# Kernel optimization log

Hardware: AMD Instinct MI355X
Metric: run time of the kernel (lower is better)

Reference implementation:

```python
import jax, jax.numpy as jnp
import numpy as np

B, S, H, L, C = 32, 512, 768, 512, 3  # batch, seq, hidden, max_length, num_classes


def _lin_init(k, fan_in, shape):
    return jax.random.normal(k, shape, jnp.float32) * (1.0 / np.sqrt(fan_in))


def setup_inputs() -> dict:
    key = jax.random.key(0)
    ks = jax.random.split(key, 18)
    return {
        "tokens": jax.random.normal(ks[0], (B, S, H), jnp.float32),
        # shared Q/K/V projections (used for both token- and feature-attention)
        "Wq": _lin_init(ks[1], H, (H, H)), "bq": jnp.zeros((H,), jnp.float32),
        "Wk": _lin_init(ks[2], H, (H, H)), "bk": jnp.zeros((H,), jnp.float32),
        "Wv": _lin_init(ks[3], H, (H, H)), "bv": jnp.zeros((H,), jnp.float32),
        # TSGSA: Linear(H,1)+ReLU gate over tokens
        "W_ts": _lin_init(ks[4], H, (H, 1)), "b_ts": jnp.zeros((1,), jnp.float32),
        # FSGSA: Linear(max_length,1)+ReLU gate over padded seq axis (also reused for FGSA per source bug)
        "W_fs": _lin_init(ks[5], L, (L, 1)), "b_fs": jnp.zeros((1,), jnp.float32),
        # TGSA: Linear(H,H)+Sigmoid gate
        "W_tg": _lin_init(ks[6], H, (H, H)), "b_tg": jnp.zeros((H,), jnp.float32),
        # fnn: Linear(7H,H) -> Linear(H,C)
        "W1": _lin_init(ks[7], 7 * H, (7 * H, H)), "b1": jnp.zeros((H,), jnp.float32),
        "W2": _lin_init(ks[8], H, (H, C)), "b2": jnp.zeros((C,), jnp.float32),
    }


def _ln(x):
    # LayerNorm over (seq, hidden) jointly, eps=1e-8; freshly-instantiated affine params are identity
    m = jnp.mean(x, axis=(1, 2), keepdims=True)
    v = jnp.var(x, axis=(1, 2), keepdims=True)
    return (x - m) * jax.lax.rsqrt(v + 1e-8)


def reference(tokens, Wq, bq, Wk, bk, Wv, bv, W_ts, b_ts, W_fs, b_fs, W_tg, b_tg, W1, b1, W2, b2):
    scale = 1.0 / np.sqrt(H)
    Q = tokens @ Wq + bq  # [B,S,H]
    K = tokens @ Wk + bk
    V = tokens @ Wv + bv
    # token-direction self-attention: softmax(Q K^T / sqrt(H)) V
    att = jax.nn.softmax(jnp.einsum('bsh,bth->bst', Q, K) * scale, axis=-1)  # [B,S,S]
    TSA = jnp.einsum('bst,bth->bsh', att, V)
    # feature-direction self-attention: V @ softmax(Q^T K / sqrt(H))
    attN = jax.nn.softmax(jnp.einsum('bsh,bsg->bhg', Q, K) * scale, axis=-1)  # [B,H,H]
    FSA = jnp.einsum('bsh,bhg->bsg', V, attN)
    # gate branches
    TSGSA = jax.nn.relu(tokens @ W_ts + b_ts) * tokens  # [B,S,1]*[B,S,H]
    tpad = jnp.pad(tokens.transpose(0, 2, 1), ((0, 0), (0, 0), (0, L - S)))  # [B,H,L]
    gate_f = jax.nn.relu(tpad @ W_fs + b_fs)  # [B,H,1]
    FSGSA = (gate_f * tokens.transpose(0, 2, 1)).transpose(0, 2, 1)  # [B,S,H]
    TGSA = jax.nn.sigmoid(tokens @ W_tg + b_tg) * tokens
    FGSA = FSGSA  # source bug: FGSA branch applies self.FSGSA, identical to FSGSA
    out_all = jnp.concatenate(
        [tokens, _ln(TSA), _ln(FSA), _ln(TGSA), _ln(FGSA), _ln(TSGSA), _ln(FSGSA)], axis=2)  # [B,S,7H]
    pooled = jnp.mean(out_all, axis=1)  # [B,7H]
    return (pooled @ W1 + b1) @ W2 + b2  # [B,C]
```

## Files before the change

### kernel.cpp

```cpp
#include <hip/hip_runtime.h>
#include <cmath>

typedef unsigned short u16;
typedef __attribute__((ext_vector_type(4))) float f32x4;
typedef __attribute__((ext_vector_type(4))) unsigned int u32x4;
typedef __attribute__((ext_vector_type(8))) __bf16 bf16x8;

__device__ __forceinline__ u16 f2b(float f) {
  unsigned int u = __builtin_bit_cast(unsigned int, f);
  return (u16)((u + 0x7fffu + ((u >> 16) & 1u)) >> 16);
}
__device__ __forceinline__ float b2f(u16 h) {
  unsigned int u = ((unsigned int)h) << 16;
  return __builtin_bit_cast(float, u);
}

__device__ __forceinline__ void glds16(const u16* g, u16* l) {
  __builtin_amdgcn_global_load_lds(
      (const __attribute__((address_space(1))) void*)g,
      (__attribute__((address_space(3))) void*)l, 16, 0, 0);
}

template <int EPI>
__global__ __launch_bounds__(512) void gemm_f_k(
    const u16* __restrict__ Ap, const u16* __restrict__ Bp, u16* __restrict__ Cp,
    u16* __restrict__ CpT, const float* __restrict__ bias,
    const u16* __restrict__ tokp, float* __restrict__ colsum,
    float* __restrict__ bstat, const float* __restrict__ rs, int K, int lda,
    int ldb, int ldc, long sA, long sB, long sC, float scale) {
  __shared__ alignas(16) u16 Asm[2][8192];
  __shared__ alignas(16) u16 Bsm[2][4096];
  __shared__ float scol_s[128];
  __shared__ float scrow[256];
  __shared__ float sred[2];

  const int gx = gridDim.x, gxy = gx * gridDim.y;
  const int nwg = gxy * gridDim.z;
  int orig = (blockIdx.z * gridDim.y + blockIdx.y) * gx + blockIdx.x;
  int gwi = (orig & 7) * (nwg >> 3) + (orig >> 3);
  const int z = gwi / gxy;
  int rem = gwi - z * gxy;
  const int ty = rem / gx, tx = rem - ty * gx;
  const int tileM = ty << 8, tileN = tx << 7;

  const u16* Abase = Ap + (size_t)z * sA;
  const u16* Bbase = Bp + (size_t)z * sB;

  const int tid = threadIdx.x;
  const int lane = tid & 63, w = tid >> 6;
  const int wr = (w >> 1) << 6, wc = (w & 1) << 6;
  const int fr = lane & 15, fg = lane >> 4;

  f32x4 acc[4][4];
#pragma unroll
  for (int i = 0; i < 4; ++i)
#pragma unroll
    for (int j = 0; j < 4; ++j) acc[i][j] = (f32x4){0.f, 0.f, 0.f, 0.f};

  const int sArow = (w << 5) + (lane >> 2);
  const int sBrow = (w << 4) + (lane >> 2);
  const int scol = (((lane & 3) ^ ((lane >> 3) & 3)) << 3);
  const u16* gA = Abase + (size_t)(tileM + sArow) * lda + scol;
  const u16* gB = Bbase + (size_t)(tileN + sBrow) * ldb + scol;
  const int ldsA = (w << 5) * 32;
  const int ldsB = (w << 4) * 32;

  auto STAGE = [&](int buf, int k0) {
    glds16(gA + k0, &Asm[buf][ldsA]);
    glds16(gA + (size_t)16 * lda + k0, &Asm[buf][ldsA + 512]);
    glds16(gB + k0, &Bsm[buf][ldsB]);
  };

  const int col_off = ((fg ^ ((fr >> 1) & 3)) << 3);

  const int nt = K >> 5;
  STAGE(0, 0);
  int cur = 0;
  for (int t = 0; t < nt; ++t) {
    if (t + 1 < nt) {
      STAGE(cur ^ 1, (t + 1) << 5);
      asm volatile("s_waitcnt vmcnt(3)" ::: "memory");
    } else {
      asm volatile("s_waitcnt vmcnt(0)" ::: "memory");
    }
    __builtin_amdgcn_s_barrier();
    asm volatile("" ::: "memory");
    const u16* Ab = Asm[cur];
    const u16* Bb = Bsm[cur];
    bf16x8 av[4], bw[4];
#pragma unroll
    for (int m = 0; m < 4; ++m)
      av[m] = *(const bf16x8*)&Ab[(wr + (m << 4) + fr) * 32 + col_off];
#pragma unroll
    for (int n = 0; n < 4; ++n)
      bw[n] = *(const bf16x8*)&Bb[(wc + (n << 4) + fr) * 32 + col_off];
#pragma unroll
    for (int m = 0; m < 4; ++m)
#pragma unroll
      for (int n = 0; n < 4; ++n)
        acc[m][n] =
            __builtin_amdgcn_mfma_f32_16x16x32_bf16(av[m], bw[n], acc[m][n], 0, 0, 0);
    asm volatile("" ::: "memory");
    __builtin_amdgcn_s_barrier();
    cur ^= 1;
  }

  if constexpr (EPI == 0) {
    const int cbuf = tileN / 768;
    const int nbase = tileN - cbuf * 768;
    u16* Cz = Cp + (size_t)cbuf * sC;
#pragma unroll
    for (int m = 0; m < 4; ++m) {
#pragma unroll
      for (int n = 0; n < 4; ++n) {
        const int gcol = tileN + wc + (n << 4) + fr;
        const int lcol = nbase + wc + (n << 4) + fr;
        const float bv2 = bias[gcol];
#pragma unroll
        for (int r = 0; r < 4; ++r) {
          const int grow = tileM + wr + (m << 4) + (fg << 2) + r;
          Cz[(size_t)grow * 768 + lcol] = f2b(acc[m][n][r] + bv2);
        }
      }
    }
    u16* Ct = CpT + (size_t)cbuf * sC;
    const int zb = tileM >> 9;
    const int sbase = tileM & 511;
#pragma unroll
    for (int m = 0; m < 4; ++m) {
#pragma unroll
      for (int n = 0; n < 4; ++n) {
        const int gcol = tileN + wc + (n << 4) + fr;
        const int lcol = nbase + wc + (n << 4) + fr;
        const int srow0 = sbase + wr + (m << 4) + (fg << 2);
        union { u16 u[4]; unsigned long long q; } pk;
#pragma unroll
        for (int r = 0; r < 4; ++r) pk.u[r] = f2b(acc[m][n][r] + bias[gcol]);
        *(unsigned long long*)&Ct[((size_t)(zb * 768 + lcol) << 9) + srow0] = pk.q;
      }
    }
  } else if constexpr (EPI == 1) {
    if (tid < 128) scol_s[tid] = 0.f;
    if (tid == 0) { sred[0] = 0.f; sred[1] = 0.f; }
    __syncthreads();
    float ls = 0.f, lq = 0.f;
#pragma unroll
    for (int n = 0; n < 4; ++n) {
      float cpart = 0.f;
      const int gcol = tileN + wc + (n << 4) + fr;
      const float bv2 = bias[gcol];
#pragma unroll
      for (int m = 0; m < 4; ++m) {
#pragma unroll
        for (int r = 0; r < 4; ++r) {
          const int grow = tileM + wr + (m << 4) + (fg << 2) + r;
          float g = 1.f / (1.f + __expf(-(acc[m][n][r] + bv2)));
          float v = g * b2f(tokp[(size_t)grow * 768 + gcol]);
          cpart += v; ls += v; lq += v * v;
        }
      }
      atomicAdd(&scol_s[wc + (n << 4) + fr], cpart);
    }
    atomicAdd(&sred[0], ls);
    atomicAdd(&sred[1], lq);
    __syncthreads();
    const int b = tileM >> 9;
    if (tid < 128) atomicAdd(&colsum[(size_t)b * 768 + tileN + tid], scol_s[tid]);
    if (tid == 0) {
      atomicAdd(&bstat[b], sred[0]);
      atomicAdd(&bstat[32 + b], sred[1]);
    }
  } else if constexpr (EPI == 4) {
    u16* Cz = Cp + (size_t)z * sC;
    float lsum[4];
#pragma unroll
    for (int n = 0; n < 4; ++n) {
      const int gcol = tileN + wc + (n << 4) + fr;
      float s2 = 0.f;
#pragma unroll
      for (int m = 0; m < 4; ++m) {
#pragma unroll
        for (int r = 0; r < 4; ++r) {
          const int grow = tileM + wr + (m << 4) + (fg << 2) + r;
          float e = __expf(acc[m][n][r] * scale);
          Cz[(size_t)grow * ldc + gcol] = f2b(e);
          s2 += e;
        }
      }
      lsum[n] = s2;
    }
    float* red = (float*)&Asm[0][0];
    const int slot = ((w >> 1) << 2) + fg;
    __syncthreads();
#pragma unroll
    for (int n = 0; n < 4; ++n)
      red[slot * 132 + wc + (n << 4) + fr] = lsum[n];
    __syncthreads();
    if (tid < 128) {
      float s2 = 0.f;
#pragma unroll
      for (int i = 0; i < 16; ++i) s2 += red[i * 132 + tid];
      const int ty3 = tileM >> 8;
      colsum[((size_t)z * 3 + ty3) * 768 + tileN + tid] = s2;
    }
  } else if constexpr (EPI == 5) {
    u16* Cz = Cp + (size_t)z * sC;
    if (tid < 256) scrow[tid] = 0.f;
    __syncthreads();
    float rpart[4][4];
#pragma unroll
    for (int m = 0; m < 4; ++m)
#pragma unroll
      for (int r = 0; r < 4; ++r) rpart[m][r] = 0.f;
#pragma unroll
    for (int n = 0; n < 4; ++n) {
      const int gcol = tileN + wc + (n << 4) + fr;
#pragma unroll
      for (int m = 0; m < 4; ++m) {
#pragma unroll
        for (int r = 0; r < 4; ++r) {
          const int grow = tileM + wr + (m << 4) + (fg << 2) + r;
          float e = __expf(acc[m][n][r] * scale);
          Cz[(size_t)grow * ldc + gcol] = f2b(e);
          rpart[m][r] += e;
        }
      }
    }
#pragma unroll
    for (int m = 0; m < 4; ++m) {
#pragma unroll
      for (int r = 0; r < 4; ++r) {
        float v = rpart[m][r];
        v += __shfl_xor(v, 1); v += __shfl_xor(v, 2);
        v += __shfl_xor(v, 4); v += __shfl_xor(v, 8);
        if (fr == 0) atomicAdd(&scrow[wr + (m << 4) + (fg << 2) + r], v);
      }
    }
    __syncthreads();
    if (tid < 256) atomicAdd(&colsum[(size_t)z * 512 + tileM + tid], scrow[tid]);
  } else if constexpr (EPI == 6) {
    float isr[4][4];
#pragma unroll
    for (int m = 0; m < 4; ++m)
#pragma unroll
      for (int r = 0; r < 4; ++r)
        isr[m][r] =
            1.f / rs[(size_t)z * 512 + tileM + wr + (m << 4) + (fg << 2) + r];
    if (tid < 128) scol_s[tid] = 0.f;
    if (tid == 0) { sred[0] = 0.f; sred[1] = 0.f; }
    __syncthreads();
    float ls = 0.f, lq = 0.f;
#pragma unroll
    for (int n = 0; n < 4; ++n) {
      float cpart = 0.f;
#pragma unroll
      for (int m = 0; m < 4; ++m) {
#pragma unroll
        for (int r = 0; r < 4; ++r) {
          float v = acc[m][n][r] * isr[m][r];
          cpart += v; ls += v; lq += v * v;
        }
      }
      atomicAdd(&scol_s[wc + (n << 4) + fr], cpart);
    }
    atomicAdd(&sred[0], ls);
    atomicAdd(&sred[1], lq);
    __syncthreads();
    if (tid < 128) atomicAdd(&colsum[(size_t)z * 768 + tileN + tid], scol_s[tid]);
    if (tid == 0) {
      atomicAdd(&bstat[z], sred[0]);
      atomicAdd(&bstat[32 + z], sred[1]);
    }
  } else {
    if (tid < 128) scol_s[tid] = 0.f;
    if (tid == 0) { sred[0] = 0.f; sred[1] = 0.f; }
    __syncthreads();
    float ls = 0.f, lq = 0.f;
#pragma unroll
    for (int n = 0; n < 4; ++n) {
      float cpart = 0.f;
#pragma unroll
      for (int m = 0; m < 4; ++m) {
#pragma unroll
        for (int r = 0; r < 4; ++r) {
          float v = acc[m][n][r];
          cpart += v; ls += v; lq += v * v;
        }
      }
      atomicAdd(&scol_s[wc + (n << 4) + fr], cpart);
    }
    atomicAdd(&sred[0], ls);
    atomicAdd(&sred[1], lq);
    __syncthreads();
    if (tid < 128) atomicAdd(&colsum[(size_t)z * 768 + tileN + tid], scol_s[tid]);
    if (tid == 0) {
      atomicAdd(&bstat[z], sred[0]);
      atomicAdd(&bstat[32 + z], sred[1]);
    }
  }
}

__global__ __launch_bounds__(256) void cvt_row_k(
    const float* __restrict__ tok, u16* __restrict__ tokb,
    const float* __restrict__ Wts, const float* __restrict__ bts,
    float* __restrict__ gate_t, float* __restrict__ rowsum,
    float* __restrict__ rowsumsq) {
  const int w = threadIdx.x >> 6, lane = threadIdx.x & 63;
  const int row = blockIdx.x * 4 + w;
  const float* p = tok + (size_t)row * 768;
  u16* q = tokb + (size_t)row * 768;
  float s = 0.f, sq = 0.f, g = 0.f;
#pragma unroll
  for (int i = 0; i < 3; ++i) {
    const int idx = (i * 64 + lane) << 2;
    f32x4 v = *(const f32x4*)(p + idx);
    f32x4 wv = *(const f32x4*)(Wts + idx);
    union { u16 u[4]; unsigned long long q8; } pk;
#pragma unroll
    for (int j = 0; j < 4; ++j) {
      s += v[j]; sq += v[j] * v[j]; g += v[j] * wv[j];
      pk.u[j] = f2b(v[j]);
    }
    *(unsigned long long*)(q + idx) = pk.q8;
  }
#pragma unroll
  for (int o = 32; o > 0; o >>= 1) {
    s += __shfl_xor(s, o); sq += __shfl_xor(sq, o); g += __shfl_xor(g, o);
  }
  if (lane == 0) {
    gate_t[row] = fmaxf(g + bts[0], 0.f);
    rowsum[row] = s;
    rowsumsq[row] = sq;
  }
}

__global__ __launch_bounds__(256) void transpose_w4_k(
    const float* __restrict__ W0, const float* __restrict__ W1,
    const float* __restrict__ W2, const float* __restrict__ W3,
    u16* __restrict__ WT) {
  const float* W = blockIdx.z == 0 ? W0 : blockIdx.z == 1 ? W1
                   : blockIdx.z == 2 ? W2 : W3;
  u16* dst = WT + (size_t)blockIdx.z * 589824;
  __shared__ float t[64][65];
  const int r0 = blockIdx.y << 6, c0 = blockIdx.x << 6;
  for (int i = threadIdx.x; i < 4096; i += 256) {
    int r = i >> 6, c = i & 63;
    t[r][c] = W[(size_t)(r0 + r) * 768 + c0 + c];
  }
  __syncthreads();
  for (int i = threadIdx.x; i < 4096; i += 256) {
    int rr = i >> 6, cc = i & 63;
    dst[(size_t)(c0 + rr) * 768 + r0 + cc] = f2b(t[cc][rr]);
  }
}

__global__ __launch_bounds__(256) void v2scale_k(const u16* __restrict__ Vb,
                                                 const float* __restrict__ psum,
                                                 u16* __restrict__ V2) {
  __shared__ float inv[768];
  const int z = blockIdx.x, sb = blockIdx.y;
  const float* pz = psum + (size_t)z * 2304;
  for (int h = threadIdx.x; h < 768; h += 256)
    inv[h] = 1.f / (pz[h] + pz[h + 768] + pz[h + 1536]);
  __syncthreads();
  const size_t base = (size_t)z * 393216 + (size_t)sb * 64 * 768;
  for (int i = 0; i < 24; ++i) {
    const int u = i * 256 + threadIdx.x;
    const int row = u / 96, seg = (u - row * 96) * 8;
    const size_t idx = base + (size_t)row * 768 + seg;
    union { u32x4 q; u16 us[8]; } in, ot;
    in.q = *(const u32x4*)&Vb[idx];
#pragma unroll
    for (int j = 0; j < 8; ++j) ot.us[j] = f2b(b2f(in.us[j]) * inv[seg + j]);
    *(u32x4*)&V2[idx] = ot.q;
  }
}

__global__ __launch_bounds__(256) void col_stats_k(
    const u16* __restrict__ tokb, const float* __restrict__ Wfs,
    const float* __restrict__ bfs, const float* __restrict__ gate_t,
    float* __restrict__ gate_f, float* __restrict__ colsum_tok,
    float* __restrict__ colsumsq_tok, float* __restrict__ colsum_tsg) {
  const int b = blockIdx.x, h = blockIdx.y * 256 + threadIdx.x;
  const u16* p = tokb + (size_t)b * 512 * 768 + h;
  const float* gt = gate_t + b * 512;
  float cs = 0.f, cq = 0.f, gf = 0.f, tg = 0.f;
#pragma unroll 4
  for (int s = 0; s < 512; ++s) {
    float t = b2f(p[(size_t)s * 768]);
    cs += t; cq += t * t; gf += t * Wfs[s]; tg += t * gt[s];
  }
  const int idx = b * 768 + h;
  gate_f[idx] = fmaxf(gf + bfs[0], 0.f);
  colsum_tok[idx] = cs;
  colsumsq_tok[idx] = cq;
  colsum_tsg[idx] = tg;
}

__global__ __launch_bounds__(256) void batch_stats_k(
    const float* __restrict__ gate_t, const float* __restrict__ rowsum,
    const float* __restrict__ rowsumsq, const float* __restrict__ gate_f,
    const float* __restrict__ colsum_tok, const float* __restrict__ colsumsq_tok,
    float* __restrict__ st) {
  __shared__ float red[4][256];
  const int b = blockIdx.x, tid = threadIdx.x;
  float ts = 0.f, tq = 0.f, fs = 0.f, fq = 0.f;
  for (int s = tid; s < 512; s += 256) {
    float g = gate_t[b * 512 + s];
    ts += g * rowsum[b * 512 + s];
    tq += g * g * rowsumsq[b * 512 + s];
  }
  for (int h = tid; h < 768; h += 256) {
    float g = gate_f[b * 768 + h];
    fs += g * colsum_tok[b * 768 + h];
    fq += g * g * colsumsq_tok[b * 768 + h];
  }
  red[0][tid] = ts; red[1][tid] = tq; red[2][tid] = fs; red[3][tid] = fq;
  __syncthreads();
  for (int o = 128; o > 0; o >>= 1) {
    if (tid < o) {
      red[0][tid] += red[0][tid + o];
      red[1][tid] += red[1][tid + o];
      red[2][tid] += red[2][tid + o];
      red[3][tid] += red[3][tid + o];
    }
    __syncthreads();
  }
  if (tid == 0) {
    st[b] = red[0][0]; st[32 + b] = red[1][0];
    st[64 + b] = red[2][0]; st[96 + b] = red[3][0];
  }
}

__global__ __launch_bounds__(768) void pooled_k(
    const float* __restrict__ colsum_tok, const float* __restrict__ colsum_tsa,
    const float* __restrict__ bstat_tsa, const float* __restrict__ colsum_fsa,
    const float* __restrict__ bstat_fsa, const float* __restrict__ colsum_tgsa,
    const float* __restrict__ bstat_tgsa, const float* __restrict__ colsum_tsg,
    const float* __restrict__ gate_f, const float* __restrict__ st,
    float* __restrict__ pooled) {
  const int b = blockIdx.x, h = threadIdx.x;
  const float invS = 1.f / 512.f, invN = 1.f / (512.f * 768.f);
  const int i = b * 768 + h;
  float* pr = pooled + (size_t)b * 5376;
  pr[h] = colsum_tok[i] * invS;
  auto lnslot = [&](int slot, float cs, float bs, float bq) {
    float m = bs * invN;
    float var = bq * invN - m * m;
    pr[slot * 768 + h] = (cs * invS - m) * rsqrtf(var + 1e-8f);
  };
  lnslot(1, colsum_tsa[i], bstat_tsa[b], bstat_tsa[32 + b]);
  lnslot(2, colsum_fsa[i], bstat_fsa[b], bstat_fsa[32 + b]);
  lnslot(3, colsum_tgsa[i], bstat_tgsa[b], bstat_tgsa[32 + b]);
  const float fsg_cs = gate_f[i] * colsum_tok[i];
  lnslot(4, fsg_cs, st[64 + b], st[96 + b]);
  lnslot(5, colsum_tsg[i], st[b], st[32 + b]);
  lnslot(6, fsg_cs, st[64 + b], st[96 + b]);
}

__global__ __launch_bounds__(256) void fnn1_k(const float* __restrict__ pooled,
                                              const float* __restrict__ W1,
                                              float* __restrict__ tmp1) {
  __shared__ float sp[128][36];
  const int c0 = blockIdx.x << 7, k0 = blockIdx.y << 7;
  const int tid = threadIdx.x;
  for (int i = tid; i < 4096; i += 256) {
    int b = i >> 7, j = i & 127;
    sp[j][b] = pooled[(size_t)b * 5376 + k0 + j];
  }
  __syncthreads();
  const int c = c0 + (tid & 127);
  const int u = (tid >> 7) << 4;
  float acc[16];
#pragma unroll
  for (int t = 0; t < 16; ++t) acc[t] = 0.f;
#pragma unroll 4
  for (int j = 0; j < 128; ++j) {
    float w = W1[(size_t)(k0 + j) * 768 + c];
    const f32x4* row = (const f32x4*)&sp[j][u];
#pragma unroll
    for (int t4 = 0; t4 < 4; ++t4) {
      f32x4 v = row[t4];
#pragma unroll
      for (int r = 0; r < 4; ++r) acc[t4 * 4 + r] += v[r] * w;
    }
  }
#pragma unroll
  for (int t = 0; t < 16; ++t) atomicAdd(&tmp1[(u + t) * 768 + c], acc[t]);
}

__global__ __launch_bounds__(256) void fnn2_k(const float* __restrict__ tmp1,
                                              const float* __restrict__ b1,
                                              const float* __restrict__ W2,
                                              const float* __restrict__ b2,
                                              float* __restrict__ out) {
  const int gw = blockIdx.x * 4 + (threadIdx.x >> 6);
  const int lane = threadIdx.x & 63;
  const int b = gw / 3, c = gw % 3;
  float a = 0.f;
#pragma unroll
  for (int i = 0; i < 12; ++i) {
    int k = lane + i * 64;
    a += (tmp1[b * 768 + k] + b1[k]) * W2[k * 3 + c];
  }
#pragma unroll
  for (int o = 32; o > 0; o >>= 1) a += __shfl_xor(a, o);
  if (lane == 0) out[b * 3 + c] = a + b2[c];
}

extern "C" void kernel_launch(void* const* d_in, const int* in_sizes, int n_in,
                              void* d_out, int out_size, void* d_ws, size_t ws_size,
                              hipStream_t stream) {
  const float* tokens = (const float*)d_in[0];
  const float* Wq = (const float*)d_in[1];
  const float* bq = (const float*)d_in[2];
  const float* Wk = (const float*)d_in[3];
  const float* bk = (const float*)d_in[4];
  const float* Wv = (const float*)d_in[5];
  const float* bv = (const float*)d_in[6];
  const float* Wts = (const float*)d_in[7];
  const float* bts = (const float*)d_in[8];
  const float* Wfs = (const float*)d_in[9];
  const float* bfs = (const float*)d_in[10];
  const float* Wtg = (const float*)d_in[11];
  const float* btg = (const float*)d_in[12];
  const float* W1 = (const float*)d_in[13];
  const float* b1 = (const float*)d_in[14];
  const float* W2 = (const float*)d_in[15];
  const float* b2 = (const float*)d_in[16];
  float* out = (float*)d_out;

  char* ws = (char*)d_ws;
  size_t off = 0;
  auto take = [&](size_t bytes) -> char* {
    char* p = ws + off;
    off += (bytes + 255) & ~(size_t)255;
    return p;
  };
  u16* tokb = (u16*)take((size_t)16384 * 768 * 2);
  u16* WqT = (u16*)take((size_t)768 * 768 * 2);
  u16* WkT = (u16*)take((size_t)768 * 768 * 2);
  u16* WvT = (u16*)take((size_t)768 * 768 * 2);
  u16* WtgT = (u16*)take((size_t)768 * 768 * 2);
  u16* Qb = (u16*)take((size_t)16384 * 768 * 2);
  u16* Kb = (u16*)take((size_t)16384 * 768 * 2);
  u16* Vb = (u16*)take((size_t)16384 * 768 * 2);
  u16* Qt = (u16*)take((size_t)32 * 768 * 512 * 2);
  u16* Kt = (u16*)take((size_t)32 * 768 * 512 * 2);
  u16* Vt = (u16*)take((size_t)32 * 768 * 512 * 2);
  u16* attb = (u16*)take((size_t)32 * 512 * 512 * 2);
  u16* attNt = (u16*)take((size_t)32 * 768 * 768 * 2);
  float* bias3 = (float*)take(2304 * 4);
  float* psum = (float*)take((size_t)32 * 3 * 768 * 4);
  u16* V2 = Qt;
  char* zbase = ws + off;
  float* colsum_tsa = (float*)take(24576 * 4);
  float* colsum_fsa = (float*)take(24576 * 4);
  float* colsum_tgsa = (float*)take(24576 * 4);
  float* bstat_tsa = (float*)take(64 * 4);
  float* bstat_fsa = (float*)take(64 * 4);
  float* bstat_tgsa = (float*)take(64 * 4);
  float* rowsumE = (float*)take((size_t)32 * 512 * 4);
  float* tmp1 = (float*)take((size_t)32 * 768 * 4);
  size_t zbytes = (size_t)((ws + off) - zbase);
  float* colsum_tsg = (float*)take(24576 * 4);
  float* gate_t = (float*)take(16384 * 4);
  float* rowsum = (float*)take(16384 * 4);
  float* rowsumsq = (float*)take(16384 * 4);
  float* gate_f = (float*)take(24576 * 4);
  float* colsum_tok = (float*)take(24576 * 4);
  float* colsumsq_tok = (float*)take(24576 * 4);
  float* st4 = (float*)take(128 * 4);
  float* pooled = (float*)take((size_t)32 * 5376 * 4);

  hipMemsetAsync(zbase, 0, zbytes, stream);
  hipMemcpyAsync(bias3, bq, 768 * 4, hipMemcpyDeviceToDevice, stream);
  hipMemcpyAsync(bias3 + 768, bk, 768 * 4, hipMemcpyDeviceToDevice, stream);
  hipMemcpyAsync(bias3 + 1536, bv, 768 * 4, hipMemcpyDeviceToDevice, stream);

  const float scale = 1.0f / sqrtf(768.0f);
  const dim3 blk(256);
  const dim3 blk512(512);

  cvt_row_k<<<4096, blk, 0, stream>>>(tokens, tokb, Wts, bts, gate_t, rowsum,
                                      rowsumsq);
  transpose_w4_k<<<dim3(12, 12, 4), blk, 0, stream>>>(Wq, Wk, Wv, Wtg, WqT);

  gemm_f_k<0><<<dim3(18, 64, 1), blk512, 0, stream>>>(
      tokb, WqT, Qb, Qt, bias3, nullptr, nullptr, nullptr, nullptr, 768, 768,
      768, 768, 0, 0, 12582912, 0.f);
  gemm_f_k<1><<<dim3(6, 64, 1), blk512, 0, stream>>>(
      tokb, WtgT, nullptr, nullptr, btg, tokb, colsum_tgsa, bstat_tgsa, nullptr,
      768, 768, 768, 0, 0, 0, 0, 0.f);

  gemm_f_k<4><<<dim3(6, 3, 32), blk512, 0, stream>>>(
      Kt, Qt, attNt, nullptr, nullptr, nullptr, psum, nullptr, nullptr, 512,
      512, 512, 768, 393216, 393216, 589824, scale);
  v2scale_k<<<dim3(32, 8), blk, 0, stream>>>(Vb, psum, V2);

  gemm_f_k<5><<<dim3(4, 2, 32), blk512, 0, stream>>>(
      Qb, Kb, attb, nullptr, nullptr, nullptr, rowsumE, nullptr, nullptr, 768,
      768, 768, 512, 393216, 393216, 262144, scale);

  gemm_f_k<6><<<dim3(6, 2, 32), blk512, 0, stream>>>(
      attb, Vt, nullptr, nullptr, nullptr, nullptr, colsum_tsa, bstat_tsa,
      rowsumE, 512, 512, 512, 0, 262144, 393216, 0, 0.f);
  gemm_f_k<3><<<dim3(6, 2, 32), blk512, 0, stream>>>(
      V2, attNt, nullptr, nullptr, nullptr, nullptr, colsum_fsa, bstat_fsa,
      nullptr, 768, 768, 768, 0, 393216, 589824, 0, 0.f);

  col_stats_k<<<dim3(32, 3), blk, 0, stream>>>(tokb, Wfs, bfs, gate_t, gate_f,
                                               colsum_tok, colsumsq_tok, colsum_tsg);
  batch_stats_k<<<32, blk, 0, stream>>>(gate_t, rowsum, rowsumsq, gate_f,
                                        colsum_tok, colsumsq_tok, st4);

  pooled_k<<<32, 768, 0, stream>>>(colsum_tok, colsum_tsa, bstat_tsa, colsum_fsa,
                                   bstat_fsa, colsum_tgsa, bstat_tgsa, colsum_tsg,
                                   gate_f, st4, pooled);
  fnn1_k<<<dim3(6, 42), blk, 0, stream>>>(pooled, W1, tmp1);
  fnn2_k<<<24, blk, 0, stream>>>(tmp1, b1, W2, b2, out);
}
```

Baseline: 386.3 us.

## Add 256x256-tile QKV projection GEMM with 4-stage LDS pipeline

Replaces the generic EPI==0 QKV projection GEMM with a dedicated kernel that uses 256x256 output tiles (8x4 MFMA fragments per wave), a 4-deep global_load_lds ring buffer with explicit vmcnt waits, and raised wave priority around the MFMA block. Larger tiles raise arithmetic intensity and cut redundant global/LDS traffic. The deeper prefetch is meant to hide memory latency. The cost is more accumulator registers and 128KB of LDS per block, which lowers occupancy. The grid also drops to 576 blocks, which may leave some CUs unevenly loaded.

```diff
diff --git a/kernel.cpp b/kernel.cpp
--- a/kernel.cpp
+++ b/kernel.cpp
@@ -19,6 +19,122 @@
   __builtin_amdgcn_global_load_lds(
       (const __attribute__((address_space(1))) void*)g,
       (__attribute__((address_space(3))) void*)l, 16, 0, 0);
+}
+
+__global__ __launch_bounds__(512) void gemm_w_k(
+    const u16* __restrict__ Ap, const u16* __restrict__ Bp, u16* __restrict__ Cp,
+    u16* __restrict__ CpT, const float* __restrict__ bias, int K, int lda,
+    int ldb, long sC) {
+  __shared__ alignas(16) u16 smem[4][16384];
+
+  const int gx = gridDim.x;
+  const int nwg = gx * gridDim.y;
+  int orig = blockIdx.y * gx + blockIdx.x;
+  int gwi = (orig & 7) * (nwg >> 3) + (orig >> 3);
+  const int ty = gwi / gx, tx = gwi - ty * gx;
+  const int tileM = ty << 8, tileN = tx << 8;
+
+  const int tid = threadIdx.x;
+  const int lane = tid & 63, w = tid >> 6;
+  const int wm = (w >> 2) << 7;
+  const int wn = (w & 3) << 6;
+  const int fr = lane & 15, fg = lane >> 4;
+
+  f32x4 acc[8][4];
+#pragma unroll
+  for (int i = 0; i < 8; ++i)
+#pragma unroll
+    for (int j = 0; j < 4; ++j) acc[i][j] = (f32x4){0.f, 0.f, 0.f, 0.f};
+
+  const int r1 = tid >> 2, c1 = tid & 3;
+  const int r2 = r1 + 128;
+  const int sc1 = ((c1 ^ ((r1 >> 1) & 3)) << 3);
+  const int sc2 = ((c1 ^ ((r2 >> 1) & 3)) << 3);
+  const u16* gA1 = Ap + (size_t)(tileM + r1) * lda + sc1;
+  const u16* gA2 = Ap + (size_t)(tileM + r2) * lda + sc2;
+  const u16* gB1 = Bp + (size_t)(tileN + r1) * ldb + sc1;
+  const u16* gB2 = Bp + (size_t)(tileN + r2) * ldb + sc2;
+
+  auto STAGE = [&](int buf, int k0) {
+    u16* base = &smem[buf][0];
+    glds16(gA1 + k0, base + tid * 8);
+    glds16(gA2 + k0, base + (tid + 512) * 8);
+    glds16(gB1 + k0, base + 8192 + tid * 8);
+    glds16(gB2 + k0, base + 8192 + (tid + 512) * 8);
+  };
+  const int col_off = ((fg ^ ((fr >> 1) & 3)) << 3);
+
+  const int nt = K >> 5;
+  STAGE(0, 0);
+  STAGE(1, 32);
+  STAGE(2, 64);
+  asm volatile("s_waitcnt vmcnt(8)" ::: "memory");
+  __builtin_amdgcn_s_barrier();
+  for (int t = 0; t < nt; ++t) {
+    asm volatile("" ::: "memory");
+    if (t + 3 < nt) STAGE((t + 3) & 3, (t + 3) << 5);
+    const u16* Ab = &smem[t & 3][0];
+    const u16* Bb = &smem[t & 3][8192];
+    bf16x8 av[8], bw[4];
+#pragma unroll
+    for (int m = 0; m < 8; ++m)
+      av[m] = *(const bf16x8*)&Ab[(wm + (m << 4) + fr) * 32 + col_off];
+#pragma unroll
+    for (int n = 0; n < 4; ++n)
+      bw[n] = *(const bf16x8*)&Bb[(wn + (n << 4) + fr) * 32 + col_off];
+    __builtin_amdgcn_s_setprio(1);
+#pragma unroll
+    for (int m = 0; m < 8; ++m)
+#pragma unroll
+      for (int n = 0; n < 4; ++n)
+        acc[m][n] =
+            __builtin_amdgcn_mfma_f32_16x16x32_bf16(av[m], bw[n], acc[m][n], 0, 0, 0);
+    __builtin_amdgcn_s_setprio(0);
+    asm volatile("" ::: "memory");
+    if (t < nt - 1) {
+      if (t + 3 < nt)
+        asm volatile("s_waitcnt vmcnt(8)" ::: "memory");
+      else if (t + 2 < nt)
+        asm volatile("s_waitcnt vmcnt(4)" ::: "memory");
+      else
+        asm volatile("s_waitcnt vmcnt(0)" ::: "memory");
+      __builtin_amdgcn_s_barrier();
+    }
+  }
+
+  const int cbuf = tileN / 768;
+  const int nbase = tileN - cbuf * 768;
+  u16* Cz = Cp + (size_t)cbuf * sC;
+#pragma unroll
+  for (int m = 0; m < 8; ++m) {
+#pragma unroll
+    for (int n = 0; n < 4; ++n) {
+      const int gcol = tileN + wn + (n << 4) + fr;
+      const int lcol = nbase + wn + (n << 4) + fr;
+      const float bv2 = bias[gcol];
+#pragma unroll
+      for (int r = 0; r < 4; ++r) {
+        const int grow = tileM + wm + (m << 4) + (fg << 2) + r;
+        Cz[(size_t)grow * 768 + lcol] = f2b(acc[m][n][r] + bv2);
+      }
+    }
+  }
+  u16* Ct = CpT + (size_t)cbuf * sC;
+  const int zb = tileM >> 9;
+  const int sbase = tileM & 511;
+#pragma unroll
+  for (int m = 0; m < 8; ++m) {
+#pragma unroll
+    for (int n = 0; n < 4; ++n) {
+      const int gcol = tileN + wn + (n << 4) + fr;
+      const int lcol = nbase + wn + (n << 4) + fr;
+      const int srow0 = sbase + wm + (m << 4) + (fg << 2);
+      union { u16 u[4]; unsigned long long q; } pk;
+#pragma unroll
+      for (int r = 0; r < 4; ++r) pk.u[r] = f2b(acc[m][n][r] + bias[gcol]);
+      *(unsigned long long*)&Ct[((size_t)(zb * 768 + lcol) << 9) + srow0] = pk.q;
+    }
+  }
 }
 
 template <int EPI>
@@ -105,41 +221,7 @@
     cur ^= 1;
   }
 
-  if constexpr (EPI == 0) {
-    const int cbuf = tileN / 768;
-    const int nbase = tileN - cbuf * 768;
-    u16* Cz = Cp + (size_t)cbuf * sC;
-#pragma unroll
-    for (int m = 0; m < 4; ++m) {
-#pragma unroll
-      for (int n = 0; n < 4; ++n) {
-        const int gcol = tileN + wc + (n << 4) + fr;
-        const int lcol = nbase + wc + (n << 4) + fr;
-        const float bv2 = bias[gcol];
-#pragma unroll
-        for (int r = 0; r < 4; ++r) {
-          const int grow = tileM + wr + (m << 4) + (fg << 2) + r;
-          Cz[(size_t)grow * 768 + lcol] = f2b(acc[m][n][r] + bv2);
-        }
-      }
-    }
-    u16* Ct = CpT + (size_t)cbuf * sC;
-    const int zb = tileM >> 9;
-    const int sbase = tileM & 511;
-#pragma unroll
-    for (int m = 0; m < 4; ++m) {
-#pragma unroll
-      for (int n = 0; n < 4; ++n) {
-        const int gcol = tileN + wc + (n << 4) + fr;
-        const int lcol = nbase + wc + (n << 4) + fr;
-        const int srow0 = sbase + wr + (m << 4) + (fg << 2);
-        union { u16 u[4]; unsigned long long q; } pk;
-#pragma unroll
-        for (int r = 0; r < 4; ++r) pk.u[r] = f2b(acc[m][n][r] + bias[gcol]);
-        *(unsigned long long*)&Ct[((size_t)(zb * 768 + lcol) << 9) + srow0] = pk.q;
-      }
-    }
-  } else if constexpr (EPI == 1) {
+  if constexpr (EPI == 1) {
     if (tid < 128) scol_s[tid] = 0.f;
     if (tid == 0) { sred[0] = 0.f; sred[1] = 0.f; }
     __syncthreads();
@@ -586,9 +668,8 @@
                                       rowsumsq);
   transpose_w4_k<<<dim3(12, 12, 4), blk, 0, stream>>>(Wq, Wk, Wv, Wtg, WqT);
 
-  gemm_f_k<0><<<dim3(18, 64, 1), blk512, 0, stream>>>(
-      tokb, WqT, Qb, Qt, bias3, nullptr, nullptr, nullptr, nullptr, 768, 768,
-      768, 768, 0, 0, 12582912, 0.f);
+  gemm_w_k<<<dim3(9, 64), blk512, 0, stream>>>(tokb, WqT, Qb, Qt, bias3, 768,
+                                               768, 768, 12582912);
   gemm_f_k<1><<<dim3(6, 64, 1), blk512, 0, stream>>>(
       tokb, WtgT, nullptr, nullptr, btg, tokb, colsum_tgsa, bstat_tgsa, nullptr,
       768, 768, 768, 0, 0, 0, 0, 0.f);
```

Result: no change. 393.5 us (+1.9%).
